# Optimization experiments

Measured on AMD Instinct MI355X. Metric: run time of the kernel, lower is better.

## Reference

```python
import jax, jax.numpy as jnp
import numpy as np

E = 23   # unique experts
K = 3    # active experts per token
D = 1024 # in_features
H = 4096 # hidden_features

def setup_inputs() -> dict:
    key = jax.random.key(0)
    ks = jax.random.split(key, 8)
    s = jnp.float32(0.02)
    return {
        "x": jax.random.normal(ks[0], (4, 2048, D), jnp.float32),
        "gate_W": jax.random.normal(ks[1], (D, E), jnp.float32) * s,
        "gate_b": jnp.zeros((E,), jnp.float32),
        "W1": jax.random.normal(ks[2], (E, D, H), jnp.float32) * s,
        "b1": jnp.zeros((E, H), jnp.float32),
        "W2": jax.random.normal(ks[3], (E, H, D), jnp.float32) * s,
        "b2": jnp.zeros((E, D), jnp.float32),
        "sW1": jax.random.normal(ks[4], (D, H), jnp.float32) * s,
        "sb1": jnp.zeros((H,), jnp.float32),
        "sW2": jax.random.normal(ks[5], (H, D), jnp.float32) * s,
        "sb2": jnp.zeros((D,), jnp.float32),
        "bias": jnp.zeros((E,), jnp.float32),  # registered buffer, zeros
    }

def _mlp(x, w1, bb1, w2, bb2):
    # torch nn.GELU default is exact (erf) GELU; drop=0 so dropout is identity
    return jax.nn.gelu(x @ w1 + bb1, approximate=False) @ w2 + bb2

def reference(x, gate_W, gate_b, W1, b1, W2, b2, sW1, sb1, sW2, sb2, bias):
    oshape = x.shape
    xf = x.reshape(-1, oshape[-1])            # [N, D]
    N = xf.shape[0]
    gw = jax.nn.sigmoid(xf @ gate_W + gate_b) # [N, E]
    # top-k selected on (gate + bias), weights gathered from raw gate
    _, topi = jax.lax.top_k(gw + bias, K)     # [N, K]
    topw = jnp.take_along_axis(gw, topi, axis=-1)
    topw = topw / topw.sum(-1, keepdims=True)
    # dense [N, E] combine-weight matrix (0 for unselected experts);
    # per-token topk indices are distinct so .set is safe
    wmat = jnp.zeros((N, E), gw.dtype).at[jnp.arange(N)[:, None], topi].set(topw)
    shared = _mlp(xf, sW1, sb1, sW2, sb2)     # shared expert over all tokens
    # scan over the 23 experts, accumulating weighted expert outputs.
    # (jit-friendly stand-in for the variable-size dispatch/grouped-GEMM.)
    def body(acc, ws):
        w1, bb1, w2, bb2, wcol = ws
        return acc + wcol[:, None] * _mlp(xf, w1, bb1, w2, bb2), None
    out, _ = jax.lax.scan(body, shared, (W1, b1, W2, b2, wmat.T))
    # load-balance auxiliary loss
    counts = jnp.zeros((E,), jnp.float32).at[topi.reshape(-1)].add(1.0)
    P = (gw / gw.sum(-1, keepdims=True)).mean(0)
    Fload = E * counts / (K * N)
    return out.reshape(oshape), (P * Fload).sum()
```

## Files before the change

kernel.cpp:

```cpp
#include <hip/hip_runtime.h>
#include <math.h>

#define DD 1024
#define HH 4096
#define EE 23
#define KK 3
#define NTOK 8192
#define BM 128
#define BN 128
#define BK 32
#define MAXROWS 35712
#define MAXTILES 280

typedef unsigned short u16;
typedef __attribute__((ext_vector_type(8))) short bf16x8;
typedef __attribute__((ext_vector_type(8))) unsigned short u16x8;
typedef __attribute__((ext_vector_type(4))) float f32x4;
typedef __attribute__((address_space(3))) unsigned int lds_u32;
typedef const __attribute__((address_space(1))) unsigned int gbl_u32;

struct Tile { int rowStart; int validEnd; int expert; };

__device__ __forceinline__ u16 f2bf(float f) {
    unsigned int u = __float_as_uint(f);
    unsigned int r = 0x7FFFu + ((u >> 16) & 1u);
    return (u16)((u + r) >> 16);
}
__device__ __forceinline__ float gelu_exact(float x) {
    float z = x * 0.70710678118654752f;
    float a = fabsf(z);
    float t = __builtin_amdgcn_rcpf(1.0f + 0.3275911f * a);
    float e = __builtin_amdgcn_exp2f(-a * a * 1.4426950408889634f);
    float p = t * (0.254829592f + t * (-0.284496736f + t * (1.421413741f +
              t * (-1.453152027f + t * 1.061405429f))));
    float er = 1.0f - p * e;
    er = (z < 0.0f) ? -er : er;
    return 0.5f * x * (1.0f + er);
}
__device__ __forceinline__ void gl2lds16(const u16* g, u16* l) {
    __builtin_amdgcn_global_load_lds((gbl_u32*)g, (lds_u32*)l, 16, 0, 0);
}

__global__ __launch_bounds__(256) void k_transpose(
    const float* __restrict__ W1, u16* __restrict__ w1t,
    const float* __restrict__ sW1, u16* __restrict__ sw1t,
    const float* __restrict__ W2, u16* __restrict__ w2t,
    const float* __restrict__ sW2, u16* __restrict__ sw2t) {
    __shared__ float tile[64][129];
    int f = blockIdx.y, t = threadIdx.x, b = blockIdx.x;
    const float* src; u16* dst; int R, C, ct, rt;
    if (f <= EE) {
        R = DD; C = HH;
        ct = b & 31; rt = b >> 5;
        if (f == EE) { src = sW1; dst = sw1t; }
        else { size_t base = (size_t)f * DD * HH; src = W1 + base; dst = w1t + base; }
    } else {
        R = HH; C = DD;
        ct = b & 7; rt = b >> 3;
        int e = f - (EE + 1);
        if (e == EE) { src = sW2; dst = sw2t; }
        else { size_t base = (size_t)e * HH * DD; src = W2 + base; dst = w2t + base; }
    }
    int r0 = rt * 64, c0 = ct * 128;
#pragma unroll
    for (int i = 0; i < 8; i++) {
        int r = i * 8 + (t >> 5);
        int c = (t & 31) * 4;
        float4 v = *reinterpret_cast<const float4*>(&src[(size_t)(r0 + r) * C + c0 + c]);
        tile[r][c] = v.x; tile[r][c + 1] = v.y; tile[r][c + 2] = v.z; tile[r][c + 3] = v.w;
    }
    __syncthreads();
#pragma unroll
    for (int j = 0; j < 4; j++) {
        int c = j * 32 + (t >> 3);
        int r8 = (t & 7) * 8;
        u16x8 o;
#pragma unroll
        for (int k = 0; k < 8; k++) o[k] = f2bf(tile[r8 + k][c]);
        *reinterpret_cast<u16x8*>(&dst[(size_t)(c0 + c) * R + r0 + r8]) = o;
    }
}

__global__ void k_gate(const float* __restrict__ x, const float* __restrict__ gW,
                       const float* __restrict__ gb, const float* __restrict__ ebias,
                       int* __restrict__ topi, float* __restrict__ topw,
                       int* __restrict__ counts, float* __restrict__ psum,
                       u16* __restrict__ xbf) {
    int tok = blockIdx.x, t = threadIdx.x;
    float acc[EE];
#pragma unroll
    for (int e = 0; e < EE; e++) acc[e] = 0.f;
    float4 xv = reinterpret_cast<const float4*>(x + (size_t)tok * DD)[t];
    ushort4 xo;
    xo.x = f2bf(xv.x); xo.y = f2bf(xv.y); xo.z = f2bf(xv.z); xo.w = f2bf(xv.w);
    reinterpret_cast<ushort4*>(xbf + (size_t)tok * DD)[t] = xo;
    float xs[4] = {xv.x, xv.y, xv.z, xv.w};
#pragma unroll
    for (int i = 0; i < 4; i++) {
        const float* grow = gW + (size_t)(t * 4 + i) * EE;
        float xd = xs[i];
#pragma unroll
        for (int e = 0; e < EE; e++) acc[e] += xd * grow[e];
    }
#pragma unroll
    for (int e = 0; e < EE; e++) {
        float v = acc[e];
        for (int off = 32; off; off >>= 1) v += __shfl_down(v, off);
        acc[e] = v;
    }
    __shared__ float part[4][EE];
    __shared__ float gwS[EE], scoreS[EE], rowsumS;
    int wave = t >> 6, lane = t & 63;
    if (lane == 0) {
#pragma unroll
        for (int e = 0; e < EE; e++) part[wave][e] = acc[e];
    }
    __syncthreads();
    if (t < EE) {
        float v = part[0][t] + part[1][t] + part[2][t] + part[3][t] + gb[t];
        float g = 1.f / (1.f + expf(-v));
        gwS[t] = g;
        scoreS[t] = g + ebias[t];
    }
    __syncthreads();
    if (t == 0) {
        int i0 = 0, i1 = -1, i2 = -1;
        float s0 = -1e30f, s1 = -1e30f, s2 = -1e30f;
        for (int e = 0; e < EE; e++) {
            float s = scoreS[e];
            if (s > s0)      { s2 = s1; i2 = i1; s1 = s0; i1 = i0; s0 = s; i0 = e; }
            else if (s > s1) { s2 = s1; i2 = i1; s1 = s;  i1 = e; }
            else if (s > s2) { s2 = s;  i2 = e; }
        }
        float w0 = gwS[i0], w1 = gwS[i1], w2 = gwS[i2];
        float wsum = w0 + w1 + w2;
        topi[tok * 3] = i0; topi[tok * 3 + 1] = i1; topi[tok * 3 + 2] = i2;
        topw[tok * 3] = w0 / wsum; topw[tok * 3 + 1] = w1 / wsum; topw[tok * 3 + 2] = w2 / wsum;
        atomicAdd(&counts[i0], 1); atomicAdd(&counts[i1], 1); atomicAdd(&counts[i2], 1);
        float rs = 0.f;
        for (int e = 0; e < EE; e++) rs += gwS[e];
        rowsumS = rs;
    }
    __syncthreads();
    if (t < EE) atomicAdd(&psum[t], gwS[t] / rowsumS);
}

__global__ void k_setup(const int* __restrict__ counts, const float* __restrict__ psum,
                        int* __restrict__ offs, Tile* __restrict__ tiles,
                        int* __restrict__ numTiles, float* __restrict__ out_aux) {
    if (threadIdx.x != 0 || blockIdx.x != 0) return;
    int nt = 0;
    for (int i = 0; i < NTOK / BM; i++) {
        tiles[nt].rowStart = i * BM; tiles[nt].validEnd = NTOK; tiles[nt].expert = EE; nt++;
    }
    int base = NTOK;
    for (int e = 0; e < EE; e++) {
        offs[e] = base;
        int c = counts[e];
        int ntile = (c + BM - 1) / BM;
        for (int i = 0; i < ntile; i++) {
            tiles[nt].rowStart = base + i * BM; tiles[nt].validEnd = base + c; tiles[nt].expert = e; nt++;
        }
        base += ntile * BM;
    }
    numTiles[0] = nt;
    float aux = 0.f;
    for (int e = 0; e < EE; e++)
        aux += (psum[e] / (float)NTOK) * ((float)EE * (float)counts[e] / ((float)KK * (float)NTOK));
    out_aux[0] = aux;
}

__global__ void k_scatter(const int* __restrict__ topi, const float* __restrict__ topw,
                          const int* __restrict__ offs, int* __restrict__ cursor,
                          int* __restrict__ rowTok, float* __restrict__ rowW) {
    int tok = blockIdx.x * blockDim.x + threadIdx.x;
    if (tok >= NTOK) return;
    rowTok[tok] = tok; rowW[tok] = 1.0f;
    for (int k = 0; k < KK; k++) {
        int e = topi[tok * 3 + k];
        int pos = atomicAdd(&cursor[e], 1);
        int slot = offs[e] + pos;
        rowTok[slot] = tok; rowW[slot] = topw[tok * 3 + k];
    }
}

__global__ __launch_bounds__(256) void k_gemm1(
    const u16* __restrict__ xbf, const u16* __restrict__ w1t, const u16* __restrict__ sw1t,
    const float* __restrict__ b1, const float* __restrict__ sb1,
    const int* __restrict__ rowTok, const Tile* __restrict__ tiles,
    const int* __restrict__ numTiles, u16* __restrict__ hbuf, int chunkBase, int hrows) {
    const int T = MAXTILES * (HH / BN);
    int b = blockIdx.x;
    int key = (b & 7) * (T >> 3) + (b >> 3);
    int sid = key >> 5, wi = key & 31;
    int ti = (sid >> 3) * 8 + (wi >> 2);
    int p  = ((sid & 7) << 2) + (wi & 3);
    if (ti >= numTiles[0]) return;
    Tile tl = tiles[ti];
    if (tl.rowStart < chunkBase || tl.rowStart >= chunkBase + hrows) return;
    int e = tl.expert;
    const u16* wbase = (e == EE) ? sw1t : (w1t + (size_t)e * HH * DD);
    const float* bias = (e == EE) ? sb1 : (b1 + (size_t)e * HH);
    int hbase = p * BN;
    int t = threadIdx.x, lane = t & 63, wv = t >> 6, wr = wv >> 1, wc = wv & 1;

    __shared__ u16 As[BM * BK];
    __shared__ u16 Bs[BN * BK];

    int rbase = wv * 16 + (lane >> 2);
    int c8 = (lane & 3) * 8;
    int s0 = tl.rowStart + rbase, s1 = s0 + 64;
    int tA0 = (s0 < tl.validEnd) ? rowTok[s0] : 0;
    int tA1 = (s1 < tl.validEnd) ? rowTok[s1] : 0;
    const u16* a0 = xbf + (size_t)tA0 * DD + c8;
    const u16* a1 = xbf + (size_t)tA1 * DD + c8;
    const u16* g0 = wbase + (size_t)(hbase + rbase) * DD + c8;
    const u16* g1 = wbase + (size_t)(hbase + 64 + rbase) * DD + c8;
    u16* lA = &As[t * 8];
    u16* lB = &Bs[t * 8];

    f32x4 acc[4][4];
#pragma unroll
    for (int m = 0; m < 4; m++)
#pragma unroll
        for (int n = 0; n < 4; n++) acc[m][n] = (f32x4){0.f, 0.f, 0.f, 0.f};

    for (int kt = 0; kt < DD / BK; kt++) {
        __syncthreads();
        gl2lds16(a0, lA); gl2lds16(a1, lA + 2048);
        gl2lds16(g0, lB); gl2lds16(g1, lB + 2048);
        a0 += BK; a1 += BK; g0 += BK; g1 += BK;
        __syncthreads();
        bf16x8 af[4], bw[4];
#pragma unroll
        for (int m = 0; m < 4; m++)
            af[m] = *reinterpret_cast<const bf16x8*>(&As[(wr * 64 + m * 16 + (lane & 15)) * BK + (lane >> 4) * 8]);
#pragma unroll
        for (int n = 0; n < 4; n++)
            bw[n] = *reinterpret_cast<const bf16x8*>(&Bs[(wc * 64 + n * 16 + (lane & 15)) * BK + (lane >> 4) * 8]);
#pragma unroll
        for (int m = 0; m < 4; m++)
#pragma unroll
            for (int n = 0; n < 4; n++)
                acc[m][n] = __builtin_amdgcn_mfma_f32_16x16x32_bf16(af[m], bw[n], acc[m][n], 0, 0, 0);
    }

#pragma unroll
    for (int m = 0; m < 4; m++) {
        int rowl = wr * 64 + m * 16 + (lane >> 4) * 4;
#pragma unroll
        for (int r = 0; r < 4; r++) {
            int slotr = tl.rowStart + rowl + r;
            bool valid = slotr < tl.validEnd;
            size_t hoff = (size_t)(slotr - chunkBase) * HH;
#pragma unroll
            for (int n = 0; n < 4; n++) {
                int col = hbase + wc * 64 + n * 16 + (lane & 15);
                float v = acc[m][n][r] + bias[col];
                hbuf[hoff + col] = valid ? f2bf(gelu_exact(v)) : (u16)0;
            }
        }
    }
}

__global__ __launch_bounds__(256) void k_gemm2(
    const u16* __restrict__ hbuf, const u16* __restrict__ w2t, const u16* __restrict__ sw2t,
    const float* __restrict__ b2, const float* __restrict__ sb2,
    const int* __restrict__ rowTok, const float* __restrict__ rowW,
    const Tile* __restrict__ tiles, const int* __restrict__ numTiles,
    float* __restrict__ out, int chunkBase, int hrows) {
    const int T = MAXTILES * (DD / BN);
    int b = blockIdx.x;
    int key = (b & 7) * (T >> 3) + (b >> 3);
    int sid = key >> 2, wi = key & 3;
    int ti = (sid >> 2) * 2 + (wi >> 1);
    int p  = ((sid & 3) << 1) + (wi & 1);
    if (ti >= numTiles[0]) return;
    Tile tl = tiles[ti];
    if (tl.rowStart < chunkBase || tl.rowStart >= chunkBase + hrows) return;
    int e = tl.expert;
    const u16* wbase = (e == EE) ? sw2t : (w2t + (size_t)e * DD * HH);
    const float* bias = (e == EE) ? sb2 : (b2 + (size_t)e * DD);
    int dbase = p * BN;
    int t = threadIdx.x, lane = t & 63, wv = t >> 6, wr = wv >> 1, wc = wv & 1;

    __shared__ u16 As[BM * BK];
    __shared__ u16 Bs[BN * BK];

    int rbase = wv * 16 + (lane >> 2);
    int c8 = (lane & 3) * 8;
    const u16* a0 = hbuf + (size_t)(tl.rowStart - chunkBase + rbase) * HH + c8;
    const u16* a1 = hbuf + (size_t)(tl.rowStart - chunkBase + 64 + rbase) * HH + c8;
    const u16* g0 = wbase + (size_t)(dbase + rbase) * HH + c8;
    const u16* g1 = wbase + (size_t)(dbase + 64 + rbase) * HH + c8;
    u16* lA = &As[t * 8];
    u16* lB = &Bs[t * 8];

    f32x4 acc[4][4];
#pragma unroll
    for (int m = 0; m < 4; m++)
#pragma unroll
        for (int n = 0; n < 4; n++) acc[m][n] = (f32x4){0.f, 0.f, 0.f, 0.f};

    for (int kt = 0; kt < HH / BK; kt++) {
        __syncthreads();
        gl2lds16(a0, lA); gl2lds16(a1, lA + 2048);
        gl2lds16(g0, lB); gl2lds16(g1, lB + 2048);
        a0 += BK; a1 += BK; g0 += BK; g1 += BK;
        __syncthreads();
        bf16x8 af[4], bw[4];
#pragma unroll
        for (int m = 0; m < 4; m++)
            af[m] = *reinterpret_cast<const bf16x8*>(&As[(wr * 64 + m * 16 + (lane & 15)) * BK + (lane >> 4) * 8]);
#pragma unroll
        for (int n = 0; n < 4; n++)
            bw[n] = *reinterpret_cast<const bf16x8*>(&Bs[(wc * 64 + n * 16 + (lane & 15)) * BK + (lane >> 4) * 8]);
#pragma unroll
        for (int m = 0; m < 4; m++)
#pragma unroll
            for (int n = 0; n < 4; n++)
                acc[m][n] = __builtin_amdgcn_mfma_f32_16x16x32_bf16(af[m], bw[n], acc[m][n], 0, 0, 0);
    }

#pragma unroll
    for (int m = 0; m < 4; m++) {
        int rowl = wr * 64 + m * 16 + (lane >> 4) * 4;
#pragma unroll
        for (int r = 0; r < 4; r++) {
            int slotr = tl.rowStart + rowl + r;
            if (slotr < tl.validEnd) {
                int tok2 = rowTok[slotr];
                float wgt = rowW[slotr];
                float* orow = out + (size_t)tok2 * DD;
#pragma unroll
                for (int n = 0; n < 4; n++) {
                    int col = dbase + wc * 64 + n * 16 + (lane & 15);
                    float v = acc[m][n][r] + bias[col];
                    atomicAdd(&orow[col], wgt * v);
                }
            }
        }
    }
}

extern "C" void kernel_launch(void* const* d_in, const int* in_sizes, int n_in,
                              void* d_out, int out_size, void* d_ws, size_t ws_size,
                              hipStream_t stream) {
    const float* x    = (const float*)d_in[0];
    const float* gW   = (const float*)d_in[1];
    const float* gb   = (const float*)d_in[2];
    const float* W1   = (const float*)d_in[3];
    const float* b1   = (const float*)d_in[4];
    const float* W2   = (const float*)d_in[5];
    const float* b2   = (const float*)d_in[6];
    const float* sW1  = (const float*)d_in[7];
    const float* sb1  = (const float*)d_in[8];
    const float* sW2  = (const float*)d_in[9];
    const float* sb2  = (const float*)d_in[10];
    const float* ebias = (const float*)d_in[11];
    float* out = (float*)d_out;

    char* w = (char*)d_ws;
    size_t off = 0;
    auto alloc = [&](size_t bytes) -> void* {
        void* p = w + off;
        off += (bytes + 255) & ~(size_t)255;
        return p;
    };
    u16* xbf   = (u16*)alloc((size_t)NTOK * DD * 2);
    u16* w1t   = (u16*)alloc((size_t)EE * HH * DD * 2);
    u16* w2t   = (u16*)alloc((size_t)EE * DD * HH * 2);
    u16* sw1t  = (u16*)alloc((size_t)HH * DD * 2);
    u16* sw2t  = (u16*)alloc((size_t)DD * HH * 2);
    int* topi  = (int*)alloc((size_t)NTOK * 3 * 4);
    float* topw = (float*)alloc((size_t)NTOK * 3 * 4);
    int* counts = (int*)alloc(128);
    float* psum = (float*)alloc(128);
    int* cursor = (int*)alloc(128);
    int* offs   = (int*)alloc(128);
    int* rowTok = (int*)alloc((size_t)MAXROWS * 4);
    float* rowW = (float*)alloc((size_t)MAXROWS * 4);
    Tile* tiles = (Tile*)alloc((size_t)MAXTILES * sizeof(Tile));
    int* numTiles = (int*)alloc(128);

    size_t fixed = off;
    size_t remain = (ws_size > fixed) ? (ws_size - fixed) : 0;
    long hr = (long)(remain / ((size_t)HH * 2));
    if (hr > MAXROWS) hr = MAXROWS;
    hr &= ~(long)127;
    if (hr < 128) hr = 128;
    int hrows = (int)hr;
    int passes = (MAXROWS + hrows - 1) / hrows;
    u16* hbuf = (u16*)(w + fixed);

    hipMemsetAsync(d_out, 0, (size_t)NTOK * DD * 4, stream);
    hipMemsetAsync(counts, 0, 768, stream);

    k_gate<<<NTOK, 256, 0, stream>>>(x, gW, gb, ebias, topi, topw, counts, psum, xbf);
    k_transpose<<<dim3(512, 2 * (EE + 1)), 256, 0, stream>>>(
        W1, w1t, sW1, sw1t, W2, w2t, sW2, sw2t);
    k_setup<<<1, 64, 0, stream>>>(counts, psum, offs, tiles, numTiles, out + (size_t)NTOK * DD);
    k_scatter<<<NTOK / 256, 256, 0, stream>>>(topi, topw, offs, cursor, rowTok, rowW);

    for (int p = 0; p < passes; p++) {
        k_gemm1<<<MAXTILES * (HH / BN), 256, 0, stream>>>(
            xbf, w1t, sw1t, b1, sb1, rowTok, tiles, numTiles, hbuf, p * hrows, hrows);
        k_gemm2<<<MAXTILES * (DD / BN), 256, 0, stream>>>(
            hbuf, w2t, sw2t, b2, sb2, rowTok, rowW, tiles, numTiles, out, p * hrows, hrows);
    }
}
```

Baseline: 1.459 ms.

## Overlap weight transposes with gating and first GEMM via fused launches

The separate transpose kernel is split up. W1 and sW1 are transposed by extra blocks appended to the gating kernel, and W2 and sW2 are transposed by extra blocks appended to the first-pass GEMM1 launch, sharing LDS through a union. Transpose tiles shrink from 64 to 32 rows, doubling the block count. The aim is to overlap the bandwidth-bound weight conversion with compute and to remove a launch. The risk is that the transpose blocks compete with the GEMM blocks for CUs and bandwidth, and that scheduling depends on block ordering.

```diff
diff --git a/kernel.cpp b/kernel.cpp
--- a/kernel.cpp
+++ b/kernel.cpp
@@ -11,6 +11,8 @@
 #define BK 32
 #define MAXROWS 35712
 #define MAXTILES 280
+#define G1BLOCKS (MAXTILES * (HH / BN))
+#define TRBLOCKS ((EE + 1) * 1024)
 
 typedef unsigned short u16;
 typedef __attribute__((ext_vector_type(8))) short bf16x8;
@@ -41,29 +43,12 @@
     __builtin_amdgcn_global_load_lds((gbl_u32*)g, (lds_u32*)l, 16, 0, 0);
 }
 
-__global__ __launch_bounds__(256) void k_transpose(
-    const float* __restrict__ W1, u16* __restrict__ w1t,
-    const float* __restrict__ sW1, u16* __restrict__ sw1t,
-    const float* __restrict__ W2, u16* __restrict__ w2t,
-    const float* __restrict__ sW2, u16* __restrict__ sw2t) {
-    __shared__ float tile[64][129];
-    int f = blockIdx.y, t = threadIdx.x, b = blockIdx.x;
-    const float* src; u16* dst; int R, C, ct, rt;
-    if (f <= EE) {
-        R = DD; C = HH;
-        ct = b & 31; rt = b >> 5;
-        if (f == EE) { src = sW1; dst = sw1t; }
-        else { size_t base = (size_t)f * DD * HH; src = W1 + base; dst = w1t + base; }
-    } else {
-        R = HH; C = DD;
-        ct = b & 7; rt = b >> 3;
-        int e = f - (EE + 1);
-        if (e == EE) { src = sW2; dst = sw2t; }
-        else { size_t base = (size_t)e * HH * DD; src = W2 + base; dst = w2t + base; }
-    }
-    int r0 = rt * 64, c0 = ct * 128;
-#pragma unroll
-    for (int i = 0; i < 8; i++) {
+__device__ __forceinline__ void transpose_tile32(
+    float (*tile)[129], const float* __restrict__ src, u16* __restrict__ dst,
+    int R, int C, int rt, int ct, int t) {
+    int r0 = rt * 32, c0 = ct * 128;
+#pragma unroll
+    for (int i = 0; i < 4; i++) {
         int r = i * 8 + (t >> 5);
         int c = (t & 31) * 4;
         float4 v = *reinterpret_cast<const float4*>(&src[(size_t)(r0 + r) * C + c0 + c]);
@@ -71,9 +56,10 @@
     }
     __syncthreads();
 #pragma unroll
-    for (int j = 0; j < 4; j++) {
-        int c = j * 32 + (t >> 3);
-        int r8 = (t & 7) * 8;
+    for (int j = 0; j < 2; j++) {
+        int idx = j * 256 + t;
+        int c = idx >> 2;
+        int r8 = (idx & 3) * 8;
         u16x8 o;
 #pragma unroll
         for (int k = 0; k < 8; k++) o[k] = f2bf(tile[r8 + k][c]);
@@ -81,12 +67,30 @@
     }
 }
 
-__global__ void k_gate(const float* __restrict__ x, const float* __restrict__ gW,
-                       const float* __restrict__ gb, const float* __restrict__ ebias,
-                       int* __restrict__ topi, float* __restrict__ topw,
-                       int* __restrict__ counts, float* __restrict__ psum,
-                       u16* __restrict__ xbf) {
-    int tok = blockIdx.x, t = threadIdx.x;
+__global__ __launch_bounds__(256) void k_pre(
+    const float* __restrict__ x, const float* __restrict__ gW,
+    const float* __restrict__ gb, const float* __restrict__ ebias,
+    int* __restrict__ topi, float* __restrict__ topw,
+    int* __restrict__ counts, float* __restrict__ psum, u16* __restrict__ xbf,
+    const float* __restrict__ W1, u16* __restrict__ w1t,
+    const float* __restrict__ sW1, u16* __restrict__ sw1t) {
+    __shared__ float tile[32][129];
+    __shared__ float part[4][EE];
+    __shared__ float gwS[EE], scoreS[EE], rowsumS;
+    int t = threadIdx.x;
+
+    if (blockIdx.x >= NTOK) {
+        int idx = blockIdx.x - NTOK;
+        int f = idx >> 10, bb = idx & 1023;
+        int ct = bb & 31, rt = bb >> 5;
+        const float* src; u16* dst;
+        if (f == EE) { src = sW1; dst = sw1t; }
+        else { size_t base = (size_t)f * DD * HH; src = W1 + base; dst = w1t + base; }
+        transpose_tile32(tile, src, dst, DD, HH, rt, ct, t);
+        return;
+    }
+
+    int tok = blockIdx.x;
     float acc[EE];
 #pragma unroll
     for (int e = 0; e < EE; e++) acc[e] = 0.f;
@@ -108,8 +112,6 @@
         for (int off = 32; off; off >>= 1) v += __shfl_down(v, off);
         acc[e] = v;
     }
-    __shared__ float part[4][EE];
-    __shared__ float gwS[EE], scoreS[EE], rowsumS;
     int wave = t >> 6, lane = t & 63;
     if (lane == 0) {
 #pragma unroll
@@ -188,9 +190,29 @@
     const u16* __restrict__ xbf, const u16* __restrict__ w1t, const u16* __restrict__ sw1t,
     const float* __restrict__ b1, const float* __restrict__ sb1,
     const int* __restrict__ rowTok, const Tile* __restrict__ tiles,
-    const int* __restrict__ numTiles, u16* __restrict__ hbuf, int chunkBase, int hrows) {
-    const int T = MAXTILES * (HH / BN);
+    const int* __restrict__ numTiles, u16* __restrict__ hbuf, int chunkBase, int hrows,
+    const float* __restrict__ W2, u16* __restrict__ w2t,
+    const float* __restrict__ sW2, u16* __restrict__ sw2t) {
+    __shared__ union {
+        struct { u16 As[BM * BK]; u16 Bs[BN * BK]; } g;
+        float tr[32][129];
+    } sh;
+    int t = threadIdx.x;
     int b = blockIdx.x;
+
+    if (b >= G1BLOCKS) {
+        if (chunkBase != 0) return;
+        int idx = b - G1BLOCKS;
+        int f = idx >> 10, bb = idx & 1023;
+        int ct = bb & 7, rt = bb >> 3;
+        const float* src; u16* dst;
+        if (f == EE) { src = sW2; dst = sw2t; }
+        else { size_t base = (size_t)f * HH * DD; src = W2 + base; dst = w2t + base; }
+        transpose_tile32(sh.tr, src, dst, HH, DD, rt, ct, t);
+        return;
+    }
+
+    const int T = G1BLOCKS;
     int key = (b & 7) * (T >> 3) + (b >> 3);
     int sid = key >> 5, wi = key & 31;
     int ti = (sid >> 3) * 8 + (wi >> 2);
@@ -202,10 +224,7 @@
     const u16* wbase = (e == EE) ? sw1t : (w1t + (size_t)e * HH * DD);
     const float* bias = (e == EE) ? sb1 : (b1 + (size_t)e * HH);
     int hbase = p * BN;
-    int t = threadIdx.x, lane = t & 63, wv = t >> 6, wr = wv >> 1, wc = wv & 1;
-
-    __shared__ u16 As[BM * BK];
-    __shared__ u16 Bs[BN * BK];
+    int lane = t & 63, wv = t >> 6, wr = wv >> 1, wc = wv & 1;
 
     int rbase = wv * 16 + (lane >> 2);
     int c8 = (lane & 3) * 8;
@@ -216,8 +235,8 @@
     const u16* a1 = xbf + (size_t)tA1 * DD + c8;
     const u16* g0 = wbase + (size_t)(hbase + rbase) * DD + c8;
     const u16* g1 = wbase + (size_t)(hbase + 64 + rbase) * DD + c8;
-    u16* lA = &As[t * 8];
-    u16* lB = &Bs[t * 8];
+    u16* lA = &sh.g.As[t * 8];
+    u16* lB = &sh.g.Bs[t * 8];
 
     f32x4 acc[4][4];
 #pragma unroll
@@ -234,10 +253,10 @@
         bf16x8 af[4], bw[4];
 #pragma unroll
         for (int m = 0; m < 4; m++)
-            af[m] = *reinterpret_cast<const bf16x8*>(&As[(wr * 64 + m * 16 + (lane & 15)) * BK + (lane >> 4) * 8]);
+            af[m] = *reinterpret_cast<const bf16x8*>(&sh.g.As[(wr * 64 + m * 16 + (lane & 15)) * BK + (lane >> 4) * 8]);
 #pragma unroll
         for (int n = 0; n < 4; n++)
-            bw[n] = *reinterpret_cast<const bf16x8*>(&Bs[(wc * 64 + n * 16 + (lane & 15)) * BK + (lane >> 4) * 8]);
+            bw[n] = *reinterpret_cast<const bf16x8*>(&sh.g.Bs[(wc * 64 + n * 16 + (lane & 15)) * BK + (lane >> 4) * 8]);
 #pragma unroll
         for (int m = 0; m < 4; m++)
 #pragma unroll
@@ -396,15 +415,15 @@
     hipMemsetAsync(d_out, 0, (size_t)NTOK * DD * 4, stream);
     hipMemsetAsync(counts, 0, 768, stream);
 
-    k_gate<<<NTOK, 256, 0, stream>>>(x, gW, gb, ebias, topi, topw, counts, psum, xbf);
-    k_transpose<<<dim3(512, 2 * (EE + 1)), 256, 0, stream>>>(
-        W1, w1t, sW1, sw1t, W2, w2t, sW2, sw2t);
+    k_pre<<<NTOK + TRBLOCKS, 256, 0, stream>>>(
+        x, gW, gb, ebias, topi, topw, counts, psum, xbf, W1, w1t, sW1, sw1t);
     k_setup<<<1, 64, 0, stream>>>(counts, psum, offs, tiles, numTiles, out + (size_t)NTOK * DD);
     k_scatter<<<NTOK / 256, 256, 0, stream>>>(topi, topw, offs, cursor, rowTok, rowW);
 
     for (int p = 0; p < passes; p++) {
-        k_gemm1<<<MAXTILES * (HH / BN), 256, 0, stream>>>(
-            xbf, w1t, sw1t, b1, sb1, rowTok, tiles, numTiles, hbuf, p * hrows, hrows);
+        k_gemm1<<<G1BLOCKS + TRBLOCKS, 256, 0, stream>>>(
+            xbf, w1t, sw1t, b1, sb1, rowTok, tiles, numTiles, hbuf, p * hrows, hrows,
+            W2, w2t, sW2, sw2t);
         k_gemm2<<<MAXTILES * (DD / BN), 256, 0, stream>>>(
             hbuf, w2t, sw2t, b2, sb2, rowTok, rowW, tiles, numTiles, out, p * hrows, hrows);
     }
```

Result: slower. 1.953 ms (+33.9%).
